# Kernel optimization log

Hardware: AMD Instinct MI355X
Metric: run time of the kernel (lower is better)

## Reference

```python
import jax, jax.numpy as jnp
import numpy as np

NUM_HEADS = 32
NUM_KV_HEADS = 8
HEAD_DIM = 128
EPS = 1e-5
ROPE_THETA = 10000.0


def _rope(x, positions):
    # x: [S, H, D] (NeoX-style rotate-half), positions: [S] int
    half = HEAD_DIM // 2
    inv_freq = 1.0 / (ROPE_THETA ** (jnp.arange(0, HEAD_DIM, 2, dtype=jnp.float32) / HEAD_DIM))
    freqs = positions.astype(jnp.float32)[:, None] * inv_freq  # [S, half]
    cos = jnp.concatenate([jnp.cos(freqs), jnp.cos(freqs)], axis=-1)[:, None, :]  # [S,1,D]
    sin = jnp.concatenate([jnp.sin(freqs), jnp.sin(freqs)], axis=-1)[:, None, :]
    x1, x2 = x[..., :half], x[..., half:]
    rot = jnp.concatenate([-x2, x1], axis=-1)
    return x * cos + rot * sin


def setup_inputs() -> dict:
    key = jax.random.key(0)
    k1, k2, k3 = jax.random.split(key, 3)
    S, H = 2048, 4096
    q_size = NUM_HEADS * HEAD_DIM
    kv_size = NUM_KV_HEADS * HEAD_DIM
    return {
        "positions": jnp.arange(S, dtype=jnp.int32),
        "hidden_states": jax.random.normal(k1, (S, H), dtype=jnp.float32),
        "layernorm_weight": jnp.ones((H,), dtype=jnp.float32),
        "w_qkv": jax.random.normal(k2, (q_size + 2 * kv_size, H), dtype=jnp.float32) * (H ** -0.5),
        "w_o": jax.random.normal(k3, (H, q_size), dtype=jnp.float32) * (q_size ** -0.5),
    }


def reference(positions, hidden_states, layernorm_weight, w_qkv, w_o):
    S, H = hidden_states.shape
    # Fused RMSNorm (computed in f32) + QKV projection
    x32 = hidden_states.astype(jnp.float32)
    var = jnp.mean(x32 * x32, axis=-1, keepdims=True)
    xn = x32 * jax.lax.rsqrt(var + EPS) * layernorm_weight
    qkv = xn @ w_qkv.T  # [S, (Hq+2*Hkv)*D]
    q_size = NUM_HEADS * HEAD_DIM
    kv_size = NUM_KV_HEADS * HEAD_DIM
    q = qkv[:, :q_size].reshape(S, NUM_HEADS, HEAD_DIM)
    k = qkv[:, q_size:q_size + kv_size].reshape(S, NUM_KV_HEADS, HEAD_DIM)
    v = qkv[:, q_size + kv_size:].reshape(S, NUM_KV_HEADS, HEAD_DIM)
    # RoPE on q, k
    q = _rope(q, positions)
    k = _rope(k, positions)
    # GQA: expand kv heads to query heads
    group = NUM_HEADS // NUM_KV_HEADS
    k = jnp.repeat(k, group, axis=1)  # [S, Hq, D]
    v = jnp.repeat(v, group, axis=1)
    scale = HEAD_DIM ** -0.5
    scores = jnp.einsum('qhd,khd->hqk', q, k) * scale  # [Hq, S, S]
    mask = positions[:, None] >= positions[None, :]  # causal
    scores = jnp.where(mask[None, :, :], scores, jnp.finfo(scores.dtype).min)
    probs = jax.nn.softmax(scores, axis=-1)
    attn = jnp.einsum('hqk,khd->qhd', probs, v).reshape(S, q_size)
    out = attn @ w_o.T  # [S, H]
    return out.astype(hidden_states.dtype)
```

## Files before the change

kernel.cpp:

```cpp
#include <hip/hip_runtime.h>
#include <stdint.h>
#include <type_traits>


typedef __bf16 bf16x8 __attribute__((ext_vector_type(8)));
typedef float f32x4 __attribute__((ext_vector_type(4)));

#define S_LEN 2048
#define HDIM 4096
#define QKV_N 6144
#define NQH 32
#define NKVH 8
#define HD 128

__device__ __forceinline__ float bf2f(uint16_t u){
    union { uint32_t u; float f; } v; v.u = ((uint32_t)u) << 16; return v.f;
}
__device__ __forceinline__ uint16_t f2bf(float f){
    union { float f; uint32_t u; } v; v.f = f;
    uint32_t u = v.u;
    return (uint16_t)((u + 0x7FFFu + ((u >> 16) & 1u)) >> 16);
}

__device__ __forceinline__ void gload_lds16(uint16_t* lds_dst, const uint16_t* g_src){
    __builtin_amdgcn_global_load_lds(
        (const __attribute__((address_space(1))) void*)(g_src),
        (__attribute__((address_space(3))) void*)(lds_dst),
        16, 0, 0);
}

__global__ __launch_bounds__(256) void prep_k(const float* __restrict__ w_qkv,
                                              const float* __restrict__ w_o,
                                              const float* __restrict__ x,
                                              const float* __restrict__ lw,
                                              uint16_t* __restrict__ wqkv_b,
                                              uint16_t* __restrict__ wo_b,
                                              uint16_t* __restrict__ xn){
    int b = blockIdx.x;
    int t = threadIdx.x;
    if (b < 20480){
        const float* src; uint16_t* dst; size_t i;
        if (b < 12288){ src = w_qkv; dst = wqkv_b; i = (size_t)b * 2048 + t * 8; }
        else          { src = w_o;   dst = wo_b;   i = (size_t)(b - 12288) * 2048 + t * 8; }
        float4 a = *(const float4*)(src + i);
        float4 c = *(const float4*)(src + i + 4);
        uint16_t o[8];
        o[0] = f2bf(a.x); o[1] = f2bf(a.y); o[2] = f2bf(a.z); o[3] = f2bf(a.w);
        o[4] = f2bf(c.x); o[5] = f2bf(c.y); o[6] = f2bf(c.z); o[7] = f2bf(c.w);
        *(uint4*)(dst + i) = *(uint4*)o;
        return;
    }
    int row = b - 20480;
    const float* xr = x + (size_t)row * HDIM + t * 16;
    float f[16];
#pragma unroll
    for (int p = 0; p < 4; ++p) *(float4*)(f + p * 4) = *(const float4*)(xr + p * 4);
    float ss = 0.f;
#pragma unroll
    for (int i = 0; i < 16; ++i) ss += f[i] * f[i];
#pragma unroll
    for (int off = 32; off > 0; off >>= 1) ss += __shfl_down(ss, off);
    __shared__ float red[4];
    if ((t & 63) == 0) red[t >> 6] = ss;
    __syncthreads();
    float tot = red[0] + red[1] + red[2] + red[3];
    float inv = rsqrtf(tot * (1.0f / HDIM) + 1e-5f);
    float wf[16];
#pragma unroll
    for (int p = 0; p < 4; ++p) *(float4*)(wf + p * 4) = *(const float4*)(lw + t * 16 + p * 4);
    uint16_t o[16];
#pragma unroll
    for (int i = 0; i < 16; ++i) o[i] = f2bf(f[i] * inv * wf[i]);
    uint16_t* outp = xn + (size_t)row * HDIM + t * 16;
    *(uint4*)(outp)     = *(uint4*)(o);
    *(uint4*)(outp + 8) = *(uint4*)(o + 8);
}

template <typename OutT>
__global__ __launch_bounds__(256, 2) void gemm_bt_k(const uint16_t* __restrict__ A,
                                                    const uint16_t* __restrict__ B,
                                                    OutT* __restrict__ C,
                                                    int M, int N, int K){
    __shared__ uint16_t lA[128 * 64];
    __shared__ uint16_t lB[128 * 64];
    int t = threadIdx.x;
    int lane = t & 63;
    int w = t >> 6;
    int wm = w >> 1, wn = w & 1;
    int quad = lane >> 4, ln = lane & 15;
    int tileM = blockIdx.y * 128, tileN = blockIdx.x * 128;

    f32x4 acc[4][4];
#pragma unroll
    for (int i = 0; i < 4; ++i)
#pragma unroll
      for (int j = 0; j < 4; ++j) acc[i][j] = (f32x4){0.f, 0.f, 0.f, 0.f};

    for (int k0 = 0; k0 < K; k0 += 64){
        __syncthreads();
#pragma unroll
        for (int it = 0; it < 4; ++it){
            int pp = it * 256 + t;
            int row = pp >> 3, cc = pp & 7;
            int gcc = cc ^ (row & 7);
            gload_lds16(&lA[pp * 8], A + (size_t)(tileM + row) * K + k0 + gcc * 8);
            gload_lds16(&lB[pp * 8], B + (size_t)(tileN + row) * K + k0 + gcc * 8);
        }
        __syncthreads();
#pragma unroll
        for (int kk = 0; kk < 64; kk += 32){
            int cc = (kk + quad * 8) >> 3;
            bf16x8 aF[4], bF[4];
#pragma unroll
            for (int i = 0; i < 4; ++i){
                int ra = wm * 64 + i * 16 + ln;
                aF[i] = *(const bf16x8*)&lA[ra * 64 + ((cc ^ (ra & 7)) * 8)];
                int rb = wn * 64 + i * 16 + ln;
                bF[i] = *(const bf16x8*)&lB[rb * 64 + ((cc ^ (rb & 7)) * 8)];
            }
#pragma unroll
            for (int i = 0; i < 4; ++i)
#pragma unroll
                for (int j = 0; j < 4; ++j)
                    acc[i][j] = __builtin_amdgcn_mfma_f32_16x16x32_bf16(aF[i], bF[j], acc[i][j], 0, 0, 0);
        }
    }
#pragma unroll
    for (int i = 0; i < 4; ++i)
#pragma unroll
      for (int r = 0; r < 4; ++r){
          int row = tileM + wm * 64 + i * 16 + quad * 4 + r;
#pragma unroll
          for (int j = 0; j < 4; ++j){
              int col = tileN + wn * 64 + j * 16 + ln;
              if constexpr (std::is_same<OutT, float>::value)
                  C[(size_t)row * N + col] = acc[i][j][r];
              else
                  C[(size_t)row * N + col] = f2bf(acc[i][j][r]);
          }
      }
}

__global__ __launch_bounds__(256) void ropevt_k(const int* __restrict__ pos,
                                                uint16_t* __restrict__ qkv,
                                                uint16_t* __restrict__ vT){
    int b = blockIdx.x;
    int t = threadIdx.x;
    if (b < 2048){
        int s = b;
        float fpos = (float)pos[s];
        uint16_t* rowp = qkv + (size_t)s * QKV_N;
#pragma unroll
        for (int rep = 0; rep < 3; ++rep){
            int g = t + rep * 256;
            if (rep == 2 && t >= 128) break;
            int head = g >> 4;
            int i4 = (g & 15) * 4;
            int col = (head < NQH) ? head * HD : HDIM + (head - NQH) * HD;
            uint16_t* p1 = rowp + col + i4;
            uint16_t* p2 = p1 + 64;
            ushort4 u1 = *(ushort4*)p1;
            ushort4 u2 = *(ushort4*)p2;
            uint16_t e1[4] = {u1.x, u1.y, u1.z, u1.w};
            uint16_t e2[4] = {u2.x, u2.y, u2.z, u2.w};
            uint16_t o1[4], o2[4];
#pragma unroll
            for (int e = 0; e < 4; ++e){
                float j = (float)(i4 + e);
                float inv = __expf(j * -0.14391156831212787f);
                float fr = fpos * inv;
                float sn, c;
                __sincosf(fr, &sn, &c);
                float x1 = bf2f(e1[e]), x2 = bf2f(e2[e]);
                o1[e] = f2bf(x1 * c - x2 * sn);
                o2[e] = f2bf(x2 * c + x1 * sn);
            }
            *(ushort4*)p1 = make_ushort4(o1[0], o1[1], o1[2], o1[3]);
            *(ushort4*)p2 = make_ushort4(o2[0], o2[1], o2[2], o2[3]);
        }
        return;
    }
    __shared__ uint16_t tile[64][65];
    int bx = b - 2048;
    int ts = (bx & 31) * 64;
    int tc = (bx >> 5) * 64;
#pragma unroll
    for (int p = 0; p < 16; ++p){
        int lin = p * 256 + t;
        int r = lin >> 6, c = lin & 63;
        tile[r][c] = qkv[(size_t)(ts + r) * QKV_N + (HDIM + 1024) + tc + c];
    }
    __syncthreads();
#pragma unroll
    for (int p = 0; p < 16; ++p){
        int lin = p * 256 + t;
        int r = lin >> 6, c = lin & 63;
        vT[(size_t)(tc + r) * S_LEN + ts + c] = tile[c][r];
    }
}

__global__ __launch_bounds__(256, 2) void attn_k(const uint16_t* __restrict__ qkv,
                                                 const uint16_t* __restrict__ vT,
                                                 uint16_t* __restrict__ attn){
    __shared__ uint16_t lK[2][64 * 128];
    __shared__ uint16_t lV[2][64 * 128];
    __shared__ uint16_t lP[4 * 2048];
    int bid = blockIdx.x;
    int h = bid & 31;
    int z = bid >> 5;
    int qt = (z < 8) ? 15 - z : z - 8;
    int kvh = h >> 2;
    int t = threadIdx.x, lane = t & 63, w = t >> 6;
    int quad = lane >> 4, ln = lane & 15;
    int qBase = qt * 128 + w * 32;

    const float scale = 0.088388347648318447f;

    bf16x8 qF[2][4];
#pragma unroll
    for (int i = 0; i < 2; ++i)
#pragma unroll
      for (int kk = 0; kk < 4; ++kk){
          int row = qBase + i * 16 + ln;
          bf16x8 raw = *(const bf16x8*)(qkv + (size_t)row * QKV_N + h * HD + kk * 32 + quad * 8);
#pragma unroll
          for (int e = 0; e < 8; ++e){
              union { __bf16 b; uint16_t u; } cv; cv.b = raw[e];
              union { uint16_t u; __bf16 b; } cw; cw.u = f2bf(bf2f(cv.u) * scale);
              raw[e] = cw.b;
          }
          qF[i][kk] = raw;
      }

    f32x4 oAcc[2][8];
#pragma unroll
    for (int i = 0; i < 2; ++i)
#pragma unroll
      for (int j = 0; j < 8; ++j) oAcc[i][j] = (f32x4){0.f, 0.f, 0.f, 0.f};
    float lsum[2][4];
#pragma unroll
    for (int i = 0; i < 2; ++i)
#pragma unroll
      for (int r = 0; r < 4; ++r) lsum[i][r] = 0.f;

    uint16_t* pB = lP + w * 2048;

    int nkt = 2 * qt + 2;

    #define STAGE(KT, B)                                                            \
    {                                                                               \
        _Pragma("unroll")                                                           \
        for (int it = 0; it < 4; ++it){                                             \
            int pp = it * 256 + t;                                                  \
            int row = pp >> 4, cc = pp & 15;                                        \
            int gcc = cc ^ (row & 7);                                               \
            gload_lds16(&lK[B][pp * 8],                                             \
                        qkv + (size_t)((KT) * 64 + row) * QKV_N + HDIM + kvh * HD + gcc * 8); \
            int rowv = pp >> 3, ccv = pp & 7;                                       \
            int gccv = ccv ^ (rowv & 7);                                            \
            gload_lds16(&lV[B][pp * 8],                                             \
                        vT + (size_t)(kvh * HD + rowv) * S_LEN + (KT) * 64 + gccv * 8); \
        }                                                                           \
    }

    STAGE(0, 0);
    __syncthreads();

    for (int kt = 0; kt < nkt; ++kt){
        int cur = kt & 1;
        if (kt + 1 < nkt) STAGE(kt + 1, cur ^ 1);

        f32x4 sAcc[2][4];
#pragma unroll
        for (int i = 0; i < 2; ++i)
#pragma unroll
          for (int j = 0; j < 4; ++j) sAcc[i][j] = (f32x4){0.f, 0.f, 0.f, 0.f};

#pragma unroll
        for (int kk = 0; kk < 4; ++kk){
            int cc = kk * 4 + quad;
            bf16x8 bF[4];
#pragma unroll
            for (int j = 0; j < 4; ++j){
                int row = j * 16 + ln;
                bF[j] = *(const bf16x8*)&lK[cur][row * 128 + ((cc ^ (row & 7)) * 8)];
            }
#pragma unroll
            for (int i = 0; i < 2; ++i)
#pragma unroll
              for (int j = 0; j < 4; ++j)
                  sAcc[i][j] = __builtin_amdgcn_mfma_f32_16x16x32_bf16(qF[i][kk], bF[j], sAcc[i][j], 0, 0, 0);
        }

        bool diag = (kt >= nkt - 2);
#pragma unroll
        for (int i = 0; i < 2; ++i)
#pragma unroll
          for (int r = 0; r < 4; ++r){
              int qrow = qBase + i * 16 + quad * 4 + r;
              int prow = i * 16 + quad * 4 + r;
              float part = 0.f;
#pragma unroll
              for (int j = 0; j < 4; ++j){
                  float sv = sAcc[i][j][r];
                  if (diag){
                      int colg = kt * 64 + j * 16 + ln;
                      if (colg > qrow) sv = -1e30f;
                  }
                  float pv = __expf(sv);
                  part += pv;
                  int colc = j * 16 + ln;
                  pB[prow * 64 + ((((colc >> 3) ^ (prow & 7)) & 7) * 8) + (colc & 7)] = f2bf(pv);
              }
              lsum[i][r] += part;
          }

#pragma unroll
        for (int kk = 0; kk < 2; ++kk){
            int cc = kk * 4 + quad;
            bf16x8 aP[2];
#pragma unroll
            for (int i = 0; i < 2; ++i){
                int row = i * 16 + ln;
                aP[i] = *(const bf16x8*)&pB[row * 64 + (((cc ^ (row & 7)) & 7) * 8)];
            }
            bf16x8 bV[8];
#pragma unroll
            for (int j = 0; j < 8; ++j){
                int row = j * 16 + ln;
                bV[j] = *(const bf16x8*)&lV[cur][row * 64 + (((cc ^ (row & 7)) & 7) * 8)];
            }
#pragma unroll
            for (int i = 0; i < 2; ++i)
#pragma unroll
              for (int j = 0; j < 8; ++j)
                  oAcc[i][j] = __builtin_amdgcn_mfma_f32_16x16x32_bf16(aP[i], bV[j], oAcc[i][j], 0, 0, 0);
        }

        __syncthreads();
    }
    #undef STAGE

#pragma unroll
    for (int i = 0; i < 2; ++i)
#pragma unroll
      for (int r = 0; r < 4; ++r){
          float l = lsum[i][r];
#pragma unroll
          for (int off = 1; off < 16; off <<= 1) l += __shfl_xor(l, off);
          float invl = 1.0f / l;
          int row = qBase + i * 16 + quad * 4 + r;
#pragma unroll
          for (int j = 0; j < 8; ++j)
              attn[(size_t)row * HDIM + h * HD + j * 16 + ln] = f2bf(oAcc[i][j][r] * invl);
      }
}

extern "C" void kernel_launch(void* const* d_in, const int* in_sizes, int n_in,
                              void* d_out, int out_size, void* d_ws, size_t ws_size,
                              hipStream_t stream){
    const int*   positions = (const int*)d_in[0];
    const float* hidden    = (const float*)d_in[1];
    const float* lw        = (const float*)d_in[2];
    const float* w_qkv     = (const float*)d_in[3];
    const float* w_o       = (const float*)d_in[4];
    float* out = (float*)d_out;

    uint16_t* xn     = (uint16_t*)d_ws;
    uint16_t* qkv    = xn     + (size_t)S_LEN * HDIM;
    uint16_t* vT     = qkv    + (size_t)S_LEN * QKV_N;
    uint16_t* attn   = vT     + (size_t)NKVH * HD * S_LEN;
    uint16_t* wqkv_b = attn   + (size_t)S_LEN * HDIM;
    uint16_t* wo_b   = wqkv_b + (size_t)QKV_N * HDIM;

    prep_k<<<22528, 256, 0, stream>>>(w_qkv, w_o, hidden, lw, wqkv_b, wo_b, xn);
    gemm_bt_k<uint16_t><<<dim3(QKV_N / 128, S_LEN / 128), 256, 0, stream>>>(xn, wqkv_b, qkv, S_LEN, QKV_N, HDIM);
    ropevt_k<<<2560, 256, 0, stream>>>(positions, qkv, vT);
    attn_k<<<NQH * (S_LEN / 128), 256, 0, stream>>>(qkv, vT, attn);
    gemm_bt_k<float><<<dim3(HDIM / 128, S_LEN / 128), 256, 0, stream>>>(attn, wo_b, out, S_LEN, HDIM, HDIM);
}
```

Baseline: 473.1 us.

## Double-buffer GEMM LDS tiles and overlap w_o cast with attention

The GEMM kernel gets two LDS buffers, so the next K-slice is loaded with async global-to-LDS copies while MFMAs run on the current one, and one barrier per iteration is dropped. The w_o fp32-to-bf16 cast moves out of the prep kernel and into extra trailing blocks of the attention launch, so it can fill idle CUs during the unbalanced causal attention. Doubling LDS to 64KB per block may lower occupancy. The single barrier after compute must also order the prefetch writes correctly, since the global_load_lds writes are not explicitly waited on before the barrier.

```diff
diff --git a/kernel.cpp b/kernel.cpp
--- a/kernel.cpp
+++ b/kernel.cpp
@@ -29,28 +29,27 @@
         16, 0, 0);
 }
 
+__device__ __forceinline__ void cast8(const float* __restrict__ src, uint16_t* __restrict__ dst, size_t i){
+    float4 a = *(const float4*)(src + i);
+    float4 c = *(const float4*)(src + i + 4);
+    uint16_t o[8];
+    o[0] = f2bf(a.x); o[1] = f2bf(a.y); o[2] = f2bf(a.z); o[3] = f2bf(a.w);
+    o[4] = f2bf(c.x); o[5] = f2bf(c.y); o[6] = f2bf(c.z); o[7] = f2bf(c.w);
+    *(uint4*)(dst + i) = *(uint4*)o;
+}
+
 __global__ __launch_bounds__(256) void prep_k(const float* __restrict__ w_qkv,
-                                              const float* __restrict__ w_o,
                                               const float* __restrict__ x,
                                               const float* __restrict__ lw,
                                               uint16_t* __restrict__ wqkv_b,
-                                              uint16_t* __restrict__ wo_b,
                                               uint16_t* __restrict__ xn){
     int b = blockIdx.x;
     int t = threadIdx.x;
-    if (b < 20480){
-        const float* src; uint16_t* dst; size_t i;
-        if (b < 12288){ src = w_qkv; dst = wqkv_b; i = (size_t)b * 2048 + t * 8; }
-        else          { src = w_o;   dst = wo_b;   i = (size_t)(b - 12288) * 2048 + t * 8; }
-        float4 a = *(const float4*)(src + i);
-        float4 c = *(const float4*)(src + i + 4);
-        uint16_t o[8];
-        o[0] = f2bf(a.x); o[1] = f2bf(a.y); o[2] = f2bf(a.z); o[3] = f2bf(a.w);
-        o[4] = f2bf(c.x); o[5] = f2bf(c.y); o[6] = f2bf(c.z); o[7] = f2bf(c.w);
-        *(uint4*)(dst + i) = *(uint4*)o;
+    if (b < 12288){
+        cast8(w_qkv, wqkv_b, (size_t)b * 2048 + t * 8);
         return;
     }
-    int row = b - 20480;
+    int row = b - 12288;
     const float* xr = x + (size_t)row * HDIM + t * 16;
     float f[16];
 #pragma unroll
@@ -81,8 +80,8 @@
                                                     const uint16_t* __restrict__ B,
                                                     OutT* __restrict__ C,
                                                     int M, int N, int K){
-    __shared__ uint16_t lA[128 * 64];
-    __shared__ uint16_t lB[128 * 64];
+    __shared__ uint16_t lA[2][128 * 64];
+    __shared__ uint16_t lB[2][128 * 64];
     int t = threadIdx.x;
     int lane = t & 63;
     int w = t >> 6;
@@ -96,17 +95,25 @@
 #pragma unroll
       for (int j = 0; j < 4; ++j) acc[i][j] = (f32x4){0.f, 0.f, 0.f, 0.f};
 
+    #define GSTAGE(K0, BUF)                                                         \
+    {                                                                               \
+        _Pragma("unroll")                                                           \
+        for (int it = 0; it < 4; ++it){                                             \
+            int pp = it * 256 + t;                                                  \
+            int row = pp >> 3, cc = pp & 7;                                         \
+            int gcc = cc ^ (row & 7);                                               \
+            gload_lds16(&lA[BUF][pp * 8], A + (size_t)(tileM + row) * K + (K0) + gcc * 8); \
+            gload_lds16(&lB[BUF][pp * 8], B + (size_t)(tileN + row) * K + (K0) + gcc * 8); \
+        }                                                                           \
+    }
+
+    GSTAGE(0, 0);
+    __syncthreads();
+
     for (int k0 = 0; k0 < K; k0 += 64){
-        __syncthreads();
-#pragma unroll
-        for (int it = 0; it < 4; ++it){
-            int pp = it * 256 + t;
-            int row = pp >> 3, cc = pp & 7;
-            int gcc = cc ^ (row & 7);
-            gload_lds16(&lA[pp * 8], A + (size_t)(tileM + row) * K + k0 + gcc * 8);
-            gload_lds16(&lB[pp * 8], B + (size_t)(tileN + row) * K + k0 + gcc * 8);
-        }
-        __syncthreads();
+        int cur = (k0 >> 6) & 1;
+        if (k0 + 64 < K) GSTAGE(k0 + 64, cur ^ 1);
+
 #pragma unroll
         for (int kk = 0; kk < 64; kk += 32){
             int cc = (kk + quad * 8) >> 3;
@@ -114,9 +121,9 @@
 #pragma unroll
             for (int i = 0; i < 4; ++i){
                 int ra = wm * 64 + i * 16 + ln;
-                aF[i] = *(const bf16x8*)&lA[ra * 64 + ((cc ^ (ra & 7)) * 8)];
+                aF[i] = *(const bf16x8*)&lA[cur][ra * 64 + ((cc ^ (ra & 7)) * 8)];
                 int rb = wn * 64 + i * 16 + ln;
-                bF[i] = *(const bf16x8*)&lB[rb * 64 + ((cc ^ (rb & 7)) * 8)];
+                bF[i] = *(const bf16x8*)&lB[cur][rb * 64 + ((cc ^ (rb & 7)) * 8)];
             }
 #pragma unroll
             for (int i = 0; i < 4; ++i)
@@ -124,7 +131,10 @@
                 for (int j = 0; j < 4; ++j)
                     acc[i][j] = __builtin_amdgcn_mfma_f32_16x16x32_bf16(aF[i], bF[j], acc[i][j], 0, 0, 0);
         }
-    }
+        __syncthreads();
+    }
+    #undef GSTAGE
+
 #pragma unroll
     for (int i = 0; i < 4; ++i)
 #pragma unroll
@@ -201,16 +211,23 @@
 
 __global__ __launch_bounds__(256, 2) void attn_k(const uint16_t* __restrict__ qkv,
                                                  const uint16_t* __restrict__ vT,
-                                                 uint16_t* __restrict__ attn){
+                                                 uint16_t* __restrict__ attn,
+                                                 const float* __restrict__ w_o,
+                                                 uint16_t* __restrict__ wo_b){
+    int bid = blockIdx.x;
+    int t = threadIdx.x;
+    if (bid >= 512){
+        cast8(w_o, wo_b, (size_t)(bid - 512) * 2048 + t * 8);
+        return;
+    }
     __shared__ uint16_t lK[2][64 * 128];
     __shared__ uint16_t lV[2][64 * 128];
     __shared__ uint16_t lP[4 * 2048];
-    int bid = blockIdx.x;
     int h = bid & 31;
     int z = bid >> 5;
     int qt = (z < 8) ? 15 - z : z - 8;
     int kvh = h >> 2;
-    int t = threadIdx.x, lane = t & 63, w = t >> 6;
+    int lane = t & 63, w = t >> 6;
     int quad = lane >> 4, ln = lane & 15;
     int qBase = qt * 128 + w * 32;
 
@@ -373,9 +390,9 @@
     uint16_t* wqkv_b = attn   + (size_t)S_LEN * HDIM;
     uint16_t* wo_b   = wqkv_b + (size_t)QKV_N * HDIM;
 
-    prep_k<<<22528, 256, 0, stream>>>(w_qkv, w_o, hidden, lw, wqkv_b, wo_b, xn);
+    prep_k<<<14336, 256, 0, stream>>>(w_qkv, hidden, lw, wqkv_b, xn);
     gemm_bt_k<uint16_t><<<dim3(QKV_N / 128, S_LEN / 128), 256, 0, stream>>>(xn, wqkv_b, qkv, S_LEN, QKV_N, HDIM);
     ropevt_k<<<2560, 256, 0, stream>>>(positions, qkv, vT);
-    attn_k<<<NQH * (S_LEN / 128), 256, 0, stream>>>(qkv, vT, attn);
+    attn_k<<<512 + 8192, 256, 0, stream>>>(qkv, vT, attn, w_o, wo_b);
     gemm_bt_k<float><<<dim3(HDIM / 128, S_LEN / 128), 256, 0, stream>>>(attn, wo_b, out, S_LEN, HDIM, HDIM);
 }
```

Result: no change. 475.5 us (+0.5%).
